# Optimization experiments

Hardware: AMD Instinct MI355X
Metric: run time of the kernel (lower is better)

The kernel has to match this reference:

```python
import jax, jax.numpy as jnp
import numpy as np

DIM = 4096
N_HEADS = 32
N_KV_HEADS = 8
HEAD_DIM = DIM // N_HEADS  # 128
N_REP = N_HEADS // N_KV_HEADS  # 4
BSZ = 2
SEQLEN = 1024
MAX_SEQ = 1024


def setup_inputs() -> dict:
    key = jax.random.key(0)
    ks = jax.random.split(key, 8)
    x = jax.random.normal(ks[0], (BSZ, SEQLEN, DIM), dtype=jnp.float32)
    # rotary frequencies as cos/sin of the complex freqs_cis
    theta = 10000.0 ** (-jnp.arange(0, HEAD_DIM, 2, dtype=jnp.float32) / HEAD_DIM)  # (64,)
    pos = jnp.arange(SEQLEN, dtype=jnp.float32)
    ang = pos[:, None] * theta[None, :]  # (S, 64)
    freqs_cos = jnp.cos(ang)
    freqs_sin = jnp.sin(ang)
    mask = jnp.zeros((SEQLEN, MAX_SEQ), dtype=jnp.float32)
    input_indexes = jnp.arange(SEQLEN, dtype=jnp.int64) if jax.config.jax_enable_x64 else jnp.arange(SEQLEN, dtype=jnp.int32)
    s = 1.0 / np.sqrt(DIM)
    wq = jax.random.normal(ks[1], (DIM, N_HEADS * HEAD_DIM), dtype=jnp.float32) * s
    wk = jax.random.normal(ks[2], (DIM, N_KV_HEADS * HEAD_DIM), dtype=jnp.float32) * s
    wv = jax.random.normal(ks[3], (DIM, N_KV_HEADS * HEAD_DIM), dtype=jnp.float32) * s
    wo = jax.random.normal(ks[4], (N_HEADS * HEAD_DIM, DIM), dtype=jnp.float32) * s
    cache_k = jnp.zeros((BSZ, MAX_SEQ, N_KV_HEADS, HEAD_DIM), dtype=jnp.float32)
    cache_v = jnp.zeros((BSZ, MAX_SEQ, N_KV_HEADS, HEAD_DIM), dtype=jnp.float32)
    return {"x": x, "freqs_cos": freqs_cos, "freqs_sin": freqs_sin, "mask": mask,
            "input_indexes": input_indexes, "wq": wq, "wk": wk, "wv": wv, "wo": wo,
            "cache_k": cache_k, "cache_v": cache_v}


def _rope(t, cos, sin):
    # t: (B, S, H, D); rotate consecutive (even, odd) pairs as complex mult
    B, S, H, D = t.shape
    tr = t.reshape(B, S, H, D // 2, 2)
    re, im = tr[..., 0], tr[..., 1]
    c = cos[None, :, None, :]
    s = sin[None, :, None, :]
    out_re = re * c - im * s
    out_im = re * s + im * c
    return jnp.stack([out_re, out_im], axis=-1).reshape(B, S, H, D)


def reference(x, freqs_cos, freqs_sin, mask, input_indexes, wq, wk, wv, wo, cache_k, cache_v):
    B, S, _ = x.shape
    xq = (x @ wq).reshape(B, S, N_HEADS, HEAD_DIM)
    xk = (x @ wk).reshape(B, S, N_KV_HEADS, HEAD_DIM)
    xv = (x @ wv).reshape(B, S, N_KV_HEADS, HEAD_DIM)
    xq = _rope(xq, freqs_cos, freqs_sin)
    xk = _rope(xk, freqs_cos, freqs_sin)
    # KV-cache write (index_copy along time dim)
    cache_k = cache_k.at[:, input_indexes].set(xk)
    cache_v = cache_v.at[:, input_indexes].set(xv)
    # GQA attention without materializing repeated KV: group queries per kv head
    q = xq.reshape(B, S, N_KV_HEADS, N_REP, HEAD_DIM)
    scale = 1.0 / np.sqrt(HEAD_DIM)
    # scores: (B, KH, R, S, T)
    scores = jnp.einsum('bsgrd,btgd->bgrst', q, cache_k) * scale
    scores = scores + mask  # mask (S, T) broadcasts
    probs = jax.nn.softmax(scores.astype(jnp.float32), axis=-1).astype(x.dtype)
    out = jnp.einsum('bgrst,btgd->bsgrd', probs, cache_v).reshape(B, S, N_HEADS * HEAD_DIM)
    return out @ wo
```

## Files before the change

kernel.cpp:

```cpp
#include <hip/hip_runtime.h>

typedef unsigned short u16;
typedef __bf16 v8bf __attribute__((ext_vector_type(8)));
typedef float  v4f  __attribute__((ext_vector_type(4)));

static __device__ inline u16 f2bf(float f) {
    unsigned int u = __float_as_uint(f);
    unsigned int r = u + 0x7fff + ((u >> 16) & 1);
    return (u16)(r >> 16);
}

static __device__ __forceinline__ void gl2lds(const u16* g, u16* l) {
    __builtin_amdgcn_global_load_lds(
        (const __attribute__((address_space(1))) void*)g,
        (__attribute__((address_space(3))) void*)l,
        16, 0, 0);
}

__global__ __launch_bounds__(256)
void cvt_kernel(const float* __restrict__ in, u16* __restrict__ out) {
    size_t i = ((size_t)blockIdx.x * 256 + threadIdx.x) * 8;
    float4 a = *(const float4*)&in[i];
    float4 b = *(const float4*)&in[i + 4];
    ushort4 lo, hi;
    lo.x = f2bf(a.x); lo.y = f2bf(a.y); lo.z = f2bf(a.z); lo.w = f2bf(a.w);
    hi.x = f2bf(b.x); hi.y = f2bf(b.y); hi.z = f2bf(b.z); hi.w = f2bf(b.w);
    *(ushort4*)&out[i] = lo;
    *(ushort4*)&out[i + 4] = hi;
}

__global__ __launch_bounds__(256)
void transpose_cvt_kernel(const float* __restrict__ w, u16* __restrict__ wt,
                          int N, int K) {
    __shared__ __attribute__((aligned(16))) u16 Ts[64][72];
    const int k0 = blockIdx.y * 64, n0 = blockIdx.x * 64;
    const int t = threadIdx.x;
    const int rk = t >> 4, cn = (t & 15) * 4;
    #pragma unroll
    for (int p = 0; p < 4; p++) {
        float4 v = *(const float4*)&w[(size_t)(k0 + rk + p * 16) * N + n0 + cn];
        Ts[cn + 0][rk + p * 16] = f2bf(v.x);
        Ts[cn + 1][rk + p * 16] = f2bf(v.y);
        Ts[cn + 2][rk + p * 16] = f2bf(v.z);
        Ts[cn + 3][rk + p * 16] = f2bf(v.w);
    }
    __syncthreads();
    const int n = t >> 3, kc = (t & 7) * 8;
    #pragma unroll
    for (int p = 0; p < 2; p++)
        *(uint4*)&wt[(size_t)(n0 + n + p * 32) * K + k0 + kc] =
            *(const uint4*)&Ts[n + p * 32][kc];
}

__global__ __launch_bounds__(256)
void gemm_qkv(const u16* __restrict__ A, const u16* __restrict__ Bt,
              u16* __restrict__ qb, u16* __restrict__ kb, u16* __restrict__ vt,
              const float* __restrict__ fcos, const float* __restrict__ fsin,
              int K) {
    __shared__ __attribute__((aligned(16))) u16 As[128 * 32];
    __shared__ __attribute__((aligned(16))) u16 Bs[128 * 32];
    const int tid  = threadIdx.x;
    const int m0   = blockIdx.y * 128;
    const int n0   = blockIdx.x * 128;
    const int wave = tid >> 6;
    const int lane = tid & 63;
    const int quad = lane >> 4;
    const int l16  = lane & 15;
    const int wm   = (wave >> 1) * 64;
    const int wn   = (wave & 1) * 64;
    const int lrow = lane >> 2;
    const int lch  = (lane & 3) * 8;

    v4f acc[4][4];
    #pragma unroll
    for (int i = 0; i < 4; i++)
        #pragma unroll
        for (int j = 0; j < 4; j++)
            acc[i][j] = v4f{0.f, 0.f, 0.f, 0.f};

    for (int k0 = 0; k0 < K; k0 += 32) {
        #pragma unroll
        for (int p = 0; p < 2; p++) {
            int rbase = p * 64 + wave * 16;
            gl2lds(&A[(size_t)(m0 + rbase + lrow) * K + k0 + lch], &As[rbase * 32]);
            gl2lds(&Bt[(size_t)(n0 + rbase + lrow) * K + k0 + lch], &Bs[rbase * 32]);
        }
        __syncthreads();
        v8bf a[4], b[4];
        #pragma unroll
        for (int i = 0; i < 4; i++)
            a[i] = *(const v8bf*)&As[(wm + i * 16 + l16) * 32 + quad * 8];
        #pragma unroll
        for (int j = 0; j < 4; j++)
            b[j] = *(const v8bf*)&Bs[(wn + j * 16 + l16) * 32 + quad * 8];
        #pragma unroll
        for (int i = 0; i < 4; i++)
            #pragma unroll
            for (int j = 0; j < 4; j++)
                acc[i][j] = __builtin_amdgcn_mfma_f32_16x16x32_bf16(a[i], b[j], acc[i][j], 0, 0, 0);
        __syncthreads();
    }

    const bool isV = (n0 >= 5120);
    const bool isK = (n0 >= 4096) && !isV;
    u16* outp = isK ? kb : qb;
    const int ldc   = isK ? 1024 : 4096;
    const int cbase = isK ? 4096 : 0;
    const bool odd = l16 & 1;

    #pragma unroll
    for (int i = 0; i < 4; i++) {
        #pragma unroll
        for (int j = 0; j < 4; j++) {
            const int col  = n0 + wn + j * 16 + l16;
            const int row0 = m0 + wm + i * 16 + quad * 4;
            if (isV) {
                const int gd = col - 5120;
                const int b  = row0 >> 10, tt = row0 & 1023;
                ushort4 o;
                o.x = f2bf(acc[i][j][0]); o.y = f2bf(acc[i][j][1]);
                o.z = f2bf(acc[i][j][2]); o.w = f2bf(acc[i][j][3]);
                *(ushort4*)&vt[(size_t)b * 1048576 + (size_t)gd * 1024 + tt] = o;
            } else {
                const int ii = (col & 127) >> 1;
                #pragma unroll
                for (int r = 0; r < 4; r++) {
                    float val = acc[i][j][r];
                    float other = __shfl_xor(val, 1);
                    int s = (row0 + r) & 1023;
                    float c  = fcos[s * 64 + ii];
                    float sn = fsin[s * 64 + ii];
                    float o = odd ? fmaf(other, sn, val * c)
                                  : fmaf(val, c, -(other * sn));
                    outp[(size_t)(row0 + r) * ldc + (col - cbase)] = f2bf(o);
                }
            }
        }
    }
}

__global__ __launch_bounds__(256)
void gemm_wo(const u16* __restrict__ A, const u16* __restrict__ Bt,
             float* __restrict__ C, int M, int N, int K) {
    __shared__ __attribute__((aligned(16))) u16 As[128 * 32];
    __shared__ __attribute__((aligned(16))) u16 Bs[128 * 32];
    const int tid  = threadIdx.x;
    const int m0   = blockIdx.y * 128;
    const int n0   = blockIdx.x * 128;
    const int wave = tid >> 6;
    const int lane = tid & 63;
    const int quad = lane >> 4;
    const int l16  = lane & 15;
    const int wm   = (wave >> 1) * 64;
    const int wn   = (wave & 1) * 64;
    const int lrow = lane >> 2;
    const int lch  = (lane & 3) * 8;

    v4f acc[4][4];
    #pragma unroll
    for (int i = 0; i < 4; i++)
        #pragma unroll
        for (int j = 0; j < 4; j++)
            acc[i][j] = v4f{0.f, 0.f, 0.f, 0.f};

    for (int k0 = 0; k0 < K; k0 += 32) {
        #pragma unroll
        for (int p = 0; p < 2; p++) {
            int rbase = p * 64 + wave * 16;
            gl2lds(&A[(size_t)(m0 + rbase + lrow) * K + k0 + lch], &As[rbase * 32]);
            gl2lds(&Bt[(size_t)(n0 + rbase + lrow) * K + k0 + lch], &Bs[rbase * 32]);
        }
        __syncthreads();
        v8bf a[4], b[4];
        #pragma unroll
        for (int i = 0; i < 4; i++)
            a[i] = *(const v8bf*)&As[(wm + i * 16 + l16) * 32 + quad * 8];
        #pragma unroll
        for (int j = 0; j < 4; j++)
            b[j] = *(const v8bf*)&Bs[(wn + j * 16 + l16) * 32 + quad * 8];
        #pragma unroll
        for (int i = 0; i < 4; i++)
            #pragma unroll
            for (int j = 0; j < 4; j++)
                acc[i][j] = __builtin_amdgcn_mfma_f32_16x16x32_bf16(a[i], b[j], acc[i][j], 0, 0, 0);
        __syncthreads();
    }

    #pragma unroll
    for (int i = 0; i < 4; i++)
        #pragma unroll
        for (int j = 0; j < 4; j++) {
            const int col  = n0 + wn + j * 16 + l16;
            const int row0 = m0 + wm + i * 16 + quad * 4;
            #pragma unroll
            for (int r = 0; r < 4; r++)
                C[(size_t)(row0 + r) * N + col] = acc[i][j][r];
        }
}

__global__ __launch_bounds__(256)
void attn_kernel(const u16* __restrict__ q, const u16* __restrict__ k,
                 const u16* __restrict__ vt, u16* __restrict__ out) {
    __shared__ __attribute__((aligned(16))) u16 Qs[64 * 136];
    __shared__ __attribute__((aligned(16))) u16 Ks[64 * 136];
    __shared__ __attribute__((aligned(16))) u16 Vs[128 * 72];
    __shared__ __attribute__((aligned(16))) u16 Ps[4 * 16 * 72];

    const int tid  = threadIdx.x;
    const int qt   = blockIdx.x;
    const int bh   = blockIdx.y;
    const int b    = bh >> 5;
    const int h    = bh & 31;
    const int g    = h >> 2;
    const int wave = tid >> 6, lane = tid & 63, quad = lane >> 4, l16 = lane & 15;
    const int wq0  = wave * 16;
    const int g8   = tid & 15;
    const int trow = tid >> 4;

    const size_t qbase = ((size_t)b * 1024) * 4096 + (size_t)h * 128;
    const size_t kbase = ((size_t)b * 1024) * 1024 + (size_t)g * 128;
    const size_t vtb   = (size_t)b * 1048576 + (size_t)g * 131072;
    const float kscale = 0.08838834764831845f * 1.4426950408889634f;

    #pragma unroll
    for (int p = 0; p < 4; p++) {
        int r = trow + p * 16;
        *(uint4*)&Qs[r * 136 + g8 * 8] =
            *(const uint4*)&q[qbase + (size_t)(qt * 64 + r) * 4096 + g8 * 8];
    }

    float l_run[4] = {0.f, 0.f, 0.f, 0.f};
    v4f O[8];
    #pragma unroll
    for (int df = 0; df < 8; df++) O[df] = v4f{0.f, 0.f, 0.f, 0.f};

    u16* Pw = &Ps[wave * 16 * 72];

    for (int t0 = 0; t0 < 1024; t0 += 64) {
        __syncthreads();
        #pragma unroll
        for (int p = 0; p < 4; p++) {
            int r = trow + p * 16;
            *(uint4*)&Ks[r * 136 + g8 * 8] =
                *(const uint4*)&k[kbase + (size_t)(t0 + r) * 1024 + g8 * 8];
        }
        #pragma unroll
        for (int p = 0; p < 4; p++) {
            int d = (tid >> 3) + p * 32;
            int toff = (tid & 7) * 8;
            *(uint4*)&Vs[d * 72 + toff] =
                *(const uint4*)&vt[vtb + (size_t)d * 1024 + t0 + toff];
        }
        __syncthreads();

        v4f sfrag[4];
        #pragma unroll
        for (int jn = 0; jn < 4; jn++) sfrag[jn] = v4f{0.f, 0.f, 0.f, 0.f};
        #pragma unroll
        for (int ks = 0; ks < 4; ks++) {
            v8bf af = *(const v8bf*)&Qs[(wq0 + l16) * 136 + ks * 32 + quad * 8];
            #pragma unroll
            for (int jn = 0; jn < 4; jn++) {
                v8bf bf = *(const v8bf*)&Ks[(jn * 16 + l16) * 136 + ks * 32 + quad * 8];
                sfrag[jn] = __builtin_amdgcn_mfma_f32_16x16x32_bf16(af, bf, sfrag[jn], 0, 0, 0);
            }
        }

        #pragma unroll
        for (int jn = 0; jn < 4; jn++)
            #pragma unroll
            for (int r = 0; r < 4; r++) {
                float pv = __builtin_amdgcn_exp2f(sfrag[jn][r] * kscale);
                l_run[r] += pv;
                Pw[(quad * 4 + r) * 72 + jn * 16 + l16] = f2bf(pv);
            }

        #pragma unroll
        for (int ts = 0; ts < 2; ts++) {
            v8bf pf = *(const v8bf*)&Pw[l16 * 72 + ts * 32 + quad * 8];
            #pragma unroll
            for (int df = 0; df < 8; df++) {
                v8bf vf = *(const v8bf*)&Vs[(df * 16 + l16) * 72 + ts * 32 + quad * 8];
                O[df] = __builtin_amdgcn_mfma_f32_16x16x32_bf16(pf, vf, O[df], 0, 0, 0);
            }
        }
    }

    #pragma unroll
    for (int off = 1; off < 16; off <<= 1)
        #pragma unroll
        for (int r = 0; r < 4; r++)
            l_run[r] += __shfl_xor(l_run[r], off, 64);
    float inv[4];
    #pragma unroll
    for (int r = 0; r < 4; r++) inv[r] = __builtin_amdgcn_rcpf(l_run[r]);

    const size_t obase = ((size_t)b * 1024 + qt * 64 + wq0 + quad * 4) * 4096 + (size_t)h * 128;
    #pragma unroll
    for (int df = 0; df < 8; df++)
        #pragma unroll
        for (int r = 0; r < 4; r++)
            out[obase + (size_t)r * 4096 + df * 16 + l16] = f2bf(O[df][r] * inv[r]);
}

extern "C" void kernel_launch(void* const* d_in, const int* in_sizes, int n_in,
                              void* d_out, int out_size, void* d_ws, size_t ws_size,
                              hipStream_t stream) {
    const float* x    = (const float*)d_in[0];
    const float* fcos = (const float*)d_in[1];
    const float* fsin = (const float*)d_in[2];
    const float* wq   = (const float*)d_in[5];
    const float* wk   = (const float*)d_in[6];
    const float* wv   = (const float*)d_in[7];
    const float* wo   = (const float*)d_in[8];

    u16* xb = (u16*)d_ws;
    u16* Wt = xb + (size_t)2048 * 4096;
    u16* qb = Wt + (size_t)6144 * 4096;
    u16* kb = qb + (size_t)2048 * 4096;
    u16* vb = kb + (size_t)2048 * 1024;
    u16* ab = xb;

    dim3 blk(256);
    cvt_kernel<<<dim3(4096), blk, 0, stream>>>(x, xb);
    transpose_cvt_kernel<<<dim3(64, 64), blk, 0, stream>>>(wq, Wt, 4096, 4096);
    transpose_cvt_kernel<<<dim3(16, 64), blk, 0, stream>>>(wk, Wt + (size_t)4096 * 4096, 1024, 4096);
    transpose_cvt_kernel<<<dim3(16, 64), blk, 0, stream>>>(wv, Wt + (size_t)5120 * 4096, 1024, 4096);
    gemm_qkv<<<dim3(48, 16), blk, 0, stream>>>(xb, Wt, qb, kb, vb, fcos, fsin, 4096);
    attn_kernel<<<dim3(16, 64), blk, 0, stream>>>(qb, kb, vb, ab);
    transpose_cvt_kernel<<<dim3(64, 64), blk, 0, stream>>>(wo, Wt, 4096, 4096);
    gemm_wo<<<dim3(32, 16), blk, 0, stream>>>(ab, Wt, (float*)d_out, 2048, 4096, 4096);
}
```

Measured before the change: 537.6 us.

## Map attention blocks to KV groups so four heads share K/V tiles

Each attention block now processes one KV group with one query head per wave and 32 query rows, instead of one head per block. Each K/V tile loaded into LDS is reused by all four heads of the group, which cuts global and LDS K/V traffic. Q fragments are held in registers rather than LDS, and each wave computes two 16-row tiles. This raises register use (doubled O accumulators and score fragments), which may limit occupancy.

```diff
diff --git a/kernel.cpp b/kernel.cpp
--- a/kernel.cpp
+++ b/kernel.cpp
@@ -198,43 +198,46 @@
         }
 }
 
-__global__ __launch_bounds__(256)
+__global__ __launch_bounds__(256, 2)
 void attn_kernel(const u16* __restrict__ q, const u16* __restrict__ k,
                  const u16* __restrict__ vt, u16* __restrict__ out) {
-    __shared__ __attribute__((aligned(16))) u16 Qs[64 * 136];
     __shared__ __attribute__((aligned(16))) u16 Ks[64 * 136];
     __shared__ __attribute__((aligned(16))) u16 Vs[128 * 72];
-    __shared__ __attribute__((aligned(16))) u16 Ps[4 * 16 * 72];
+    __shared__ __attribute__((aligned(16))) u16 Ps[4 * 32 * 72];
 
     const int tid  = threadIdx.x;
     const int qt   = blockIdx.x;
-    const int bh   = blockIdx.y;
-    const int b    = bh >> 5;
-    const int h    = bh & 31;
-    const int g    = h >> 2;
+    const int bg   = blockIdx.y;
+    const int b    = bg >> 3;
+    const int g    = bg & 7;
     const int wave = tid >> 6, lane = tid & 63, quad = lane >> 4, l16 = lane & 15;
-    const int wq0  = wave * 16;
+    const int h    = g * 4 + wave;
     const int g8   = tid & 15;
     const int trow = tid >> 4;
 
-    const size_t qbase = ((size_t)b * 1024) * 4096 + (size_t)h * 128;
     const size_t kbase = ((size_t)b * 1024) * 1024 + (size_t)g * 128;
     const size_t vtb   = (size_t)b * 1048576 + (size_t)g * 131072;
     const float kscale = 0.08838834764831845f * 1.4426950408889634f;
 
-    #pragma unroll
-    for (int p = 0; p < 4; p++) {
-        int r = trow + p * 16;
-        *(uint4*)&Qs[r * 136 + g8 * 8] =
-            *(const uint4*)&q[qbase + (size_t)(qt * 64 + r) * 4096 + g8 * 8];
-    }
-
-    float l_run[4] = {0.f, 0.f, 0.f, 0.f};
-    v4f O[8];
-    #pragma unroll
-    for (int df = 0; df < 8; df++) O[df] = v4f{0.f, 0.f, 0.f, 0.f};
-
-    u16* Pw = &Ps[wave * 16 * 72];
+    v8bf qf[2][4];
+    {
+        const size_t qrow = (size_t)b * 1024 + (size_t)qt * 32;
+        #pragma unroll
+        for (int rt = 0; rt < 2; rt++)
+            #pragma unroll
+            for (int ks = 0; ks < 4; ks++)
+                qf[rt][ks] = *(const v8bf*)&q[(qrow + rt * 16 + l16) * 4096 +
+                                              h * 128 + ks * 32 + quad * 8];
+    }
+
+    float l_run[2][4] = {{0.f,0.f,0.f,0.f},{0.f,0.f,0.f,0.f}};
+    v4f O[2][8];
+    #pragma unroll
+    for (int rt = 0; rt < 2; rt++)
+        #pragma unroll
+        for (int df = 0; df < 8; df++) O[rt][df] = v4f{0.f, 0.f, 0.f, 0.f};
+
+    u16* Pw = &Ps[wave * 32 * 72];
 
     for (int t0 = 0; t0 < 1024; t0 += 64) {
         __syncthreads();
@@ -253,35 +256,41 @@
         }
         __syncthreads();
 
-        v4f sfrag[4];
-        #pragma unroll
-        for (int jn = 0; jn < 4; jn++) sfrag[jn] = v4f{0.f, 0.f, 0.f, 0.f};
+        v4f sfrag[2][4];
+        #pragma unroll
+        for (int rt = 0; rt < 2; rt++)
+            #pragma unroll
+            for (int jn = 0; jn < 4; jn++) sfrag[rt][jn] = v4f{0.f, 0.f, 0.f, 0.f};
         #pragma unroll
         for (int ks = 0; ks < 4; ks++) {
-            v8bf af = *(const v8bf*)&Qs[(wq0 + l16) * 136 + ks * 32 + quad * 8];
             #pragma unroll
             for (int jn = 0; jn < 4; jn++) {
                 v8bf bf = *(const v8bf*)&Ks[(jn * 16 + l16) * 136 + ks * 32 + quad * 8];
-                sfrag[jn] = __builtin_amdgcn_mfma_f32_16x16x32_bf16(af, bf, sfrag[jn], 0, 0, 0);
+                sfrag[0][jn] = __builtin_amdgcn_mfma_f32_16x16x32_bf16(qf[0][ks], bf, sfrag[0][jn], 0, 0, 0);
+                sfrag[1][jn] = __builtin_amdgcn_mfma_f32_16x16x32_bf16(qf[1][ks], bf, sfrag[1][jn], 0, 0, 0);
             }
         }
 
         #pragma unroll
-        for (int jn = 0; jn < 4; jn++)
-            #pragma unroll
-            for (int r = 0; r < 4; r++) {
-                float pv = __builtin_amdgcn_exp2f(sfrag[jn][r] * kscale);
-                l_run[r] += pv;
-                Pw[(quad * 4 + r) * 72 + jn * 16 + l16] = f2bf(pv);
-            }
+        for (int rt = 0; rt < 2; rt++)
+            #pragma unroll
+            for (int jn = 0; jn < 4; jn++)
+                #pragma unroll
+                for (int r = 0; r < 4; r++) {
+                    float pv = __builtin_amdgcn_exp2f(sfrag[rt][jn][r] * kscale);
+                    l_run[rt][r] += pv;
+                    Pw[(rt * 16 + quad * 4 + r) * 72 + jn * 16 + l16] = f2bf(pv);
+                }
 
         #pragma unroll
         for (int ts = 0; ts < 2; ts++) {
-            v8bf pf = *(const v8bf*)&Pw[l16 * 72 + ts * 32 + quad * 8];
+            v8bf pf0 = *(const v8bf*)&Pw[(l16) * 72 + ts * 32 + quad * 8];
+            v8bf pf1 = *(const v8bf*)&Pw[(16 + l16) * 72 + ts * 32 + quad * 8];
             #pragma unroll
             for (int df = 0; df < 8; df++) {
                 v8bf vf = *(const v8bf*)&Vs[(df * 16 + l16) * 72 + ts * 32 + quad * 8];
-                O[df] = __builtin_amdgcn_mfma_f32_16x16x32_bf16(pf, vf, O[df], 0, 0, 0);
+                O[0][df] = __builtin_amdgcn_mfma_f32_16x16x32_bf16(pf0, vf, O[0][df], 0, 0, 0);
+                O[1][df] = __builtin_amdgcn_mfma_f32_16x16x32_bf16(pf1, vf, O[1][df], 0, 0, 0);
             }
         }
     }
@@ -289,18 +298,25 @@
     #pragma unroll
     for (int off = 1; off < 16; off <<= 1)
         #pragma unroll
-        for (int r = 0; r < 4; r++)
-            l_run[r] += __shfl_xor(l_run[r], off, 64);
-    float inv[4];
-    #pragma unroll
-    for (int r = 0; r < 4; r++) inv[r] = __builtin_amdgcn_rcpf(l_run[r]);
-
-    const size_t obase = ((size_t)b * 1024 + qt * 64 + wq0 + quad * 4) * 4096 + (size_t)h * 128;
-    #pragma unroll
-    for (int df = 0; df < 8; df++)
-        #pragma unroll
-        for (int r = 0; r < 4; r++)
-            out[obase + (size_t)r * 4096 + df * 16 + l16] = f2bf(O[df][r] * inv[r]);
+        for (int rt = 0; rt < 2; rt++)
+            #pragma unroll
+            for (int r = 0; r < 4; r++)
+                l_run[rt][r] += __shfl_xor(l_run[rt][r], off, 64);
+    float inv[2][4];
+    #pragma unroll
+    for (int rt = 0; rt < 2; rt++)
+        #pragma unroll
+        for (int r = 0; r < 4; r++) inv[rt][r] = __builtin_amdgcn_rcpf(l_run[rt][r]);
+
+    const size_t orow = (size_t)b * 1024 + (size_t)qt * 32;
+    #pragma unroll
+    for (int rt = 0; rt < 2; rt++)
+        #pragma unroll
+        for (int df = 0; df < 8; df++)
+            #pragma unroll
+            for (int r = 0; r < 4; r++)
+                out[(orow + rt * 16 + quad * 4 + r) * 4096 + h * 128 + df * 16 + l16] =
+                    f2bf(O[rt][df][r] * inv[rt][r]);
 }
 
 extern "C" void kernel_launch(void* const* d_in, const int* in_sizes, int n_in,
@@ -327,7 +343,7 @@
     transpose_cvt_kernel<<<dim3(16, 64), blk, 0, stream>>>(wk, Wt + (size_t)4096 * 4096, 1024, 4096);
     transpose_cvt_kernel<<<dim3(16, 64), blk, 0, stream>>>(wv, Wt + (size_t)5120 * 4096, 1024, 4096);
     gemm_qkv<<<dim3(48, 16), blk, 0, stream>>>(xb, Wt, qb, kb, vb, fcos, fsin, 4096);
-    attn_kernel<<<dim3(16, 64), blk, 0, stream>>>(qb, kb, vb, ab);
+    attn_kernel<<<dim3(32, 16), blk, 0, stream>>>(qb, kb, vb, ab);
     transpose_cvt_kernel<<<dim3(64, 64), blk, 0, stream>>>(wo, Wt, 4096, 4096);
     gemm_wo<<<dim3(32, 16), blk, 0, stream>>>(ab, Wt, (float*)d_out, 2048, 4096, 4096);
 }
```

After: 545.9 us. No clear change (+1.5%).
